# Kernel tuning notes

Measured on AMD Instinct MI355X. Metric: run time of the kernel, lower is better.

## Reference

```python
import jax, jax.numpy as jnp
import numpy as np

B, N, D, H = 1, 4096, 1024, 16
K = D // H
ROPE_BASE = 10000.0


def _rope_cos_sin(n, k, base, dtype):
    # GPT-NeoX style rotary embedding: inv_freq over even dims, emb = cat(freqs, freqs)
    inv_freq = 1.0 / (base ** (jnp.arange(0, k, 2, dtype=jnp.float32) / k))  # [K/2]
    pos = jnp.arange(n, dtype=jnp.float32)
    freqs = pos[:, None] * inv_freq[None, :]              # [N, K/2]
    emb = jnp.concatenate([freqs, freqs], axis=-1)        # [N, K]
    return jnp.cos(emb).astype(dtype), jnp.sin(emb).astype(dtype)


def _rotate_half(x):
    x1, x2 = jnp.split(x, 2, axis=-1)
    return jnp.concatenate([-x2, x1], axis=-1)


def setup_inputs() -> dict:
    key = jax.random.key(0)
    kx, kq, ko = jax.random.split(key, 3)
    x = jax.random.normal(kx, (B, N, D), dtype=jnp.float32)
    # torch Linear weights: [out_features, in_features], y = x @ W^T
    w_qkv = jax.random.normal(kq, (3 * H * K, D), dtype=jnp.float32) / np.sqrt(D)
    w_out = jax.random.normal(ko, (D, D), dtype=jnp.float32) / np.sqrt(D)
    return {"x": x, "w_qkv": w_qkv, "w_out": w_out}


def reference(x, w_qkv, w_out):
    b, n, d = x.shape
    qkv = jnp.einsum('bnd,ed->bne', x, w_qkv).reshape(b, n, 3, H, K)
    q, k, v = qkv[:, :, 0], qkv[:, :, 1], qkv[:, :, 2]   # [B, N, H, K]
    cos, sin = _rope_cos_sin(n, K, ROPE_BASE, x.dtype)    # [N, K]
    cos = cos[None, :, None, :]
    sin = sin[None, :, None, :]
    q = q * cos + _rotate_half(q) * sin
    k = k * cos + _rotate_half(k) * sin
    # explicit O(N^2) score matrix, as in the original module
    scores = jnp.einsum('bnhk,bmhk->bnhm', q, k) / np.sqrt(K).astype(x.dtype)
    causal_mask = jnp.tril(jnp.ones((n, n), dtype=bool))  # [N, M]
    scores = jnp.where(causal_mask[None, :, None, :], scores, jnp.finfo(x.dtype).min)
    probs = jax.nn.softmax(scores, axis=-1)
    attn = jnp.einsum('bnhm,bmhk->bnhk', probs, v).reshape(b, n, d)
    return jnp.einsum('bnd,ed->bne', attn, w_out)
```

## Files before the change

kernel.cpp:

```cpp
#include <hip/hip_runtime.h>
#include <hip/hip_bf16.h>
#include <math.h>

#define N_SEQ 4096
#define DIM   1024
#define NHEAD 16
#define HDIM  64
#define E3    3072

typedef short bf16x8 __attribute__((ext_vector_type(8)));
typedef float f32x4  __attribute__((ext_vector_type(4)));
typedef unsigned int u32;

#if __has_builtin(__builtin_amdgcn_exp2f)
#define EXP2(x) __builtin_amdgcn_exp2f(x)
#else
#define EXP2(x) exp2f(x)
#endif

__device__ __forceinline__ float bf2f(unsigned short u) {
    union { unsigned int i; float f; } x; x.i = ((unsigned int)u) << 16; return x.f;
}
__device__ __forceinline__ unsigned short f2bf(float f) {
    union { float f; unsigned int i; } x; x.f = f;
    unsigned int r = x.i + 0x7FFF + ((x.i >> 16) & 1);
    return (unsigned short)(r >> 16);
}
__device__ __forceinline__ unsigned short f2bf_fast(float f) {
    union { float f; unsigned int i; } x; x.f = f;
    return (unsigned short)((x.i + 0x8000u) >> 16);
}
__device__ __forceinline__ f32x4 mfma16(bf16x8 a, bf16x8 b, f32x4 c) {
    return __builtin_amdgcn_mfma_f32_16x16x32_bf16(a, b, c, 0, 0, 0);
}
__device__ __forceinline__ void gload_lds16(const unsigned short* g, unsigned short* l) {
    __builtin_amdgcn_global_load_lds(
        (const __attribute__((address_space(1))) u32*)g,
        (__attribute__((address_space(3))) u32*)l, 16, 0, 0);
}

__device__ __forceinline__ int probe_isf32(const unsigned short* __restrict__ X) {
    __shared__ int cnt;
    if (threadIdx.x == 0) cnt = 0;
    __syncthreads();
    int bad = 0;
    for (int i = threadIdx.x; i < 4096; i += 256) {
        float v = bf2f(X[i]);
        if (!(fabsf(v) < 1e10f)) bad = 1;
    }
    if (bad) atomicAdd(&cnt, 1);
    __syncthreads();
    return cnt > 0;
}

__global__ __launch_bounds__(256)
void prep_kernel(const void* __restrict__ X, const void* __restrict__ Wq,
                 const void* __restrict__ Wo,
                 unsigned short* __restrict__ Xb, unsigned short* __restrict__ Wqb,
                 unsigned short* __restrict__ Wob,
                 float4* __restrict__ Rt,
                 int* __restrict__ flag)
{
    const int ti = blockIdx.x * blockDim.x + threadIdx.x;
    if (ti < N_SEQ * 16) {
        const int n = ti >> 4, f = ti & 15;
        const float i0 = powf(10000.f, -((float)f)        * (1.f/32.f));
        const float i1 = powf(10000.f, -((float)(f + 16)) * (1.f/32.f));
        float s0, c0, s1, c1;
        sincosf((float)n * i0, &s0, &c0);
        sincosf((float)n * i1, &s1, &c1);
        Rt[ti] = (float4){c0, c1, s0, s1};
    }

    const int isf32 = probe_isf32((const unsigned short*)X);
    if (blockIdx.x == 0 && threadIdx.x == 0) *flag = isf32;
    if (!isf32) return;

    const int nX4  = (N_SEQ * DIM) >> 2;
    const int nWq4 = (E3 * DIM) >> 2;
    const int nWo4 = (DIM * DIM) >> 2;
    const int total = nX4 + nWq4 + nWo4;
    const int stride = gridDim.x * blockDim.x;
    for (int i = blockIdx.x * blockDim.x + threadIdx.x; i < total; i += stride) {
        const float4* src; ushort4* dst; int j = i;
        if (j < nX4)                { src = (const float4*)X  + j;  dst = (ushort4*)Xb  + j; }
        else if ((j -= nX4) < nWq4) { src = (const float4*)Wq + j;  dst = (ushort4*)Wqb + j; }
        else { j -= nWq4;             src = (const float4*)Wo + j;  dst = (ushort4*)Wob + j; }
        float4 v = *src;
        ushort4 u;
        u.x = f2bf(v.x); u.y = f2bf(v.y); u.z = f2bf(v.z); u.w = f2bf(v.w);
        *dst = u;
    }
}

__global__ __launch_bounds__(256)
void qkv_mfma_kernel(const void* __restrict__ Xo, const unsigned short* __restrict__ Xc,
                     const void* __restrict__ Wo_, const unsigned short* __restrict__ Wc,
                     const int* __restrict__ flag,
                     const float4* __restrict__ Rt,
                     unsigned short* __restrict__ Qf,
                     unsigned short* __restrict__ Kf,
                     unsigned short* __restrict__ Vf)
{
    __shared__ __align__(16) unsigned short SMEM[4][4096];

    const int isf32 = *flag;
    const unsigned short* Xb = isf32 ? Xc : (const unsigned short*)Xo;
    const unsigned short* Wb = isf32 ? Wc : (const unsigned short*)Wo_;

    const int tid  = threadIdx.x;
    const int lane = tid & 63;
    const int wave = tid >> 6;
    const int wr = wave >> 1, wc = wave & 1;
    const int lm = lane & 15, q4 = lane >> 4;
    const int rbase = blockIdx.y * 128;
    const int cbase = blockIdx.x * 128;

    const int srow = wave * 16 + (lane >> 2);
    const int scol = (lane & 3) * 8;

    const unsigned short* xsrc = Xb + (size_t)(rbase + srow) * DIM + scol;
    const unsigned short* wsrc = Wb + (size_t)(cbase + srow) * DIM + scol;
    const int la = (wr*64 + lm)*32 + q4*8;
    const int lb = (wc*64 + lm)*32 + q4*8;

    f32x4 acc[4][4];
    #pragma unroll
    for (int i = 0; i < 4; ++i)
        #pragma unroll
        for (int j = 0; j < 4; ++j) acc[i][j] = (f32x4){0.f, 0.f, 0.f, 0.f};

    #define QSTAGE(buf)                                                             \
        {                                                                           \
            _Pragma("unroll")                                                       \
            for (int j = 0; j < 2; ++j) {                                           \
                gload_lds16(xsrc + (size_t)j*64*DIM, &SMEM[buf][j*2048 + wave*512]);   \
                gload_lds16(wsrc + (size_t)j*64*DIM, &SMEM[2+buf][j*2048 + wave*512]); \
            }                                                                       \
            xsrc += 32; wsrc += 32;                                                 \
        }

    QSTAGE(0)
    for (int it = 0; it < DIM/32; ++it) {
        const int cur = it & 1;
        __syncthreads();
        if (it + 1 < DIM/32) QSTAGE(cur ^ 1)

        bf16x8 a[4], b[4];
        #pragma unroll
        for (int mi = 0; mi < 4; ++mi)
            a[mi] = *(const bf16x8*)&SMEM[cur][la + mi*512];
        #pragma unroll
        for (int ni = 0; ni < 4; ++ni)
            b[ni] = *(const bf16x8*)&SMEM[2+cur][lb + ni*512];
        #pragma unroll
        for (int mi = 0; mi < 4; ++mi)
            #pragma unroll
            for (int ni = 0; ni < 4; ++ni)
                acc[mi][ni] = mfma16(a[mi], b[ni], acc[mi][ni]);
    }
    #undef QSTAGE

    __syncthreads();

    const int ecol = cbase + wc * 64;
    const int part = ecol >> 10;
    const int h    = (ecol >> 6) & 15;
    unsigned short* ep = &SMEM[0][0] + wave*4096;

    if (part == 2) {
        #pragma unroll
        for (int mh = 0; mh < 2; ++mh) {
            #pragma unroll
            for (int mi2 = 0; mi2 < 2; ++mi2) {
                const int mi = mh*2 + mi2;
                #pragma unroll
                for (int r = 0; r < 4; ++r) {
                    const int n31 = mi2*16 + q4*4 + r;
                    #pragma unroll
                    for (int ni = 0; ni < 4; ++ni)
                        ep[(ni*16 + lm)*40 + n31] = f2bf(acc[mi][ni][r]);
                }
            }
            const int nb = rbase + wr*64 + mh*32;
            const size_t vb = (((size_t)h*128 + (nb >> 5)) << 11) + (size_t)lane*8;
            #pragma unroll
            for (int ni = 0; ni < 4; ++ni) {
                const bf16x8 fr = *(const bf16x8*)(ep + (ni*16 + lm)*40 + q4*8);
                *(bf16x8*)(Vf + vb + (size_t)ni*512) = fr;
            }
        }
    } else {
        unsigned short* dst = (part == 0) ? Qf : Kf;
        const float scl = (part == 0) ? 0.180336884f : 1.0f;
        #pragma unroll
        for (int mi = 0; mi < 4; ++mi) {
            const int tn = rbase + wr*64 + mi*16;
            #pragma unroll
            for (int r = 0; r < 4; ++r) {
                const int n = tn + q4*4 + r;
                const float4 t = Rt[(n << 4) + lm];
                const int row = (q4*4 + r)*72;
                ep[row + lm]      = f2bf((acc[mi][0][r]*t.x - acc[mi][2][r]*t.z) * scl);
                ep[row + lm + 16] = f2bf((acc[mi][1][r]*t.y - acc[mi][3][r]*t.w) * scl);
                ep[row + lm + 32] = f2bf((acc[mi][2][r]*t.x + acc[mi][0][r]*t.z) * scl);
                ep[row + lm + 48] = f2bf((acc[mi][3][r]*t.y + acc[mi][1][r]*t.w) * scl);
            }
            const size_t tb = (((size_t)(h*256 + (tn >> 4))) << 10) + (size_t)lane*8;
            #pragma unroll
            for (int c = 0; c < 2; ++c) {
                const bf16x8 fr = *(const bf16x8*)(ep + lm*72 + c*32 + q4*8);
                *(bf16x8*)(dst + tb + (size_t)c*512) = fr;
            }
        }
    }
}

__global__ __launch_bounds__(256, 2)
void attn_mfma_kernel(const unsigned short* __restrict__ Qf,
                      const unsigned short* __restrict__ Kf,
                      const unsigned short* __restrict__ Vf,
                      unsigned short* __restrict__ Attn)
{
    __shared__ __align__(16) unsigned short P16[4][2][32][40];
    __shared__ __align__(16) float Ox[2][32][64];
    __shared__ float Lx[2][32];

    const int tid  = threadIdx.x;
    const int lane = tid & 63;
    const int wave = tid >> 6;
    const int q4 = lane >> 4, lm = lane & 15;
    const int qh = wave >> 1, kh = wave & 1;

    const int h = blockIdx.x & 15;
    const int p = blockIdx.x >> 4;
    const int qwA = (p << 6) + (qh << 5);
    const int qwB = ((63 - p) << 6) + (qh << 5);
    const int ntA = p + 1;
    const int ntB = 64 - p;

    const unsigned short* qpA = Qf + (((size_t)(h*256 + (qwA >> 4))) << 10) + (size_t)lane * 8;
    const unsigned short* qpB = Qf + (((size_t)(h*256 + (qwB >> 4))) << 10) + (size_t)lane * 8;
    bf16x8 aqA[2][2], aqB[2][2];
    #pragma unroll
    for (int qi = 0; qi < 2; ++qi)
        #pragma unroll
        for (int d = 0; d < 2; ++d) {
            aqA[qi][d] = *(const bf16x8*)(qpA + qi*1024 + d*512);
            aqB[qi][d] = *(const bf16x8*)(qpB + qi*1024 + d*512);
        }

    float lA[2][4], lB[2][4];
    f32x4 oA[2][4], oB[2][4];
    #pragma unroll
    for (int qi = 0; qi < 2; ++qi) {
        #pragma unroll
        for (int r = 0; r < 4; ++r) { lA[qi][r] = 0.f; lB[qi][r] = 0.f; }
        #pragma unroll
        for (int dc = 0; dc < 4; ++dc) {
            oA[qi][dc] = (f32x4){0.f, 0.f, 0.f, 0.f};
            oB[qi][dc] = (f32x4){0.f, 0.f, 0.f, 0.f};
        }
    }

    const size_t hb = ((size_t)h) << 18;
    const unsigned short* kc = Kf + hb + (size_t)(kh*2048) + (size_t)lane*8;
    const unsigned short* vc = Vf + hb + (size_t)(kh*2048) + (size_t)lane*8;

    unsigned short* pwA  = &P16[wave][0][0][0];
    unsigned short* pwB  = &P16[wave][1][0][0];
    unsigned short* pwaA = pwA + (4*q4)*40 + lm;
    unsigned short* pwaB = pwB + (4*q4)*40 + lm;
    const unsigned short* parA = pwA + lm*40 + q4*8;
    const unsigned short* parB = pwB + lm*40 + q4*8;

    bf16x8 bk[2][2];
    bk[0][0] = *(const bf16x8*)(kc);
    bk[0][1] = *(const bf16x8*)(kc + 512);
    bk[1][0] = *(const bf16x8*)(kc + 1024);
    bk[1][1] = *(const bf16x8*)(kc + 1536);

    for (int it = 0; it < ntB; ++it) {
        const int kt = it << 6;
        const int doA = (it < ntA);

        bf16x8 bv[4];
        #pragma unroll
        for (int dc = 0; dc < 4; ++dc)
            bv[dc] = *(const bf16x8*)(vc + dc*512);

        bf16x8 nk[2][2];
        nk[0][0] = *(const bf16x8*)(kc + 4096);
        nk[0][1] = *(const bf16x8*)(kc + 4096 + 512);
        nk[1][0] = *(const bf16x8*)(kc + 4096 + 1024);
        nk[1][1] = *(const bf16x8*)(kc + 4096 + 1536);

        f32x4 sB[2][2], sA[2][2];
        #pragma unroll
        for (int ki = 0; ki < 2; ++ki)
            #pragma unroll
            for (int qi = 0; qi < 2; ++qi) {
                f32x4 z = (f32x4){0.f, 0.f, 0.f, 0.f};
                z = mfma16(aqB[qi][0], bk[ki][0], z);
                sB[qi][ki] = mfma16(aqB[qi][1], bk[ki][1], z);
            }
        if (doA) {
            #pragma unroll
            for (int ki = 0; ki < 2; ++ki)
                #pragma unroll
                for (int qi = 0; qi < 2; ++qi) {
                    f32x4 z = (f32x4){0.f, 0.f, 0.f, 0.f};
                    z = mfma16(aqA[qi][0], bk[ki][0], z);
                    sA[qi][ki] = mfma16(aqA[qi][1], bk[ki][1], z);
                }
        }

        if (kt + 32*kh + 31 > qwB) {
            #pragma unroll
            for (int ki = 0; ki < 2; ++ki) {
                const int key = kt + 32*kh + 16*ki + lm;
                #pragma unroll
                for (int qi = 0; qi < 2; ++qi) {
                    const int qq = qwB + 16*qi + 4*q4;
                    #pragma unroll
                    for (int r = 0; r < 4; ++r)
                        if (key > qq + r) sB[qi][ki][r] = -INFINITY;
                }
            }
        }

        #pragma unroll
        for (int qi = 0; qi < 2; ++qi)
            #pragma unroll
            for (int ki = 0; ki < 2; ++ki)
                #pragma unroll
                for (int r = 0; r < 4; ++r) {
                    const float pb = EXP2(sB[qi][ki][r]);
                    lB[qi][r] += pb;
                    pwaB[qi*640 + r*40 + ki*16] = f2bf_fast(pb);
                }

        if (doA) {
            if (kt + 32*kh + 31 > qwA) {
                #pragma unroll
                for (int ki = 0; ki < 2; ++ki) {
                    const int key = kt + 32*kh + 16*ki + lm;
                    #pragma unroll
                    for (int qi = 0; qi < 2; ++qi) {
                        const int qq = qwA + 16*qi + 4*q4;
                        #pragma unroll
                        for (int r = 0; r < 4; ++r)
                            if (key > qq + r) sA[qi][ki][r] = -INFINITY;
                    }
                }
            }
            #pragma unroll
            for (int qi = 0; qi < 2; ++qi)
                #pragma unroll
                for (int ki = 0; ki < 2; ++ki)
                    #pragma unroll
                    for (int r = 0; r < 4; ++r) {
                        const float pa = EXP2(sA[qi][ki][r]);
                        lA[qi][r] += pa;
                        pwaA[qi*640 + r*40 + ki*16] = f2bf_fast(pa);
                    }
        }

        {
            bf16x8 paB[2];
            paB[0] = *(const bf16x8*)(parB);
            paB[1] = *(const bf16x8*)(parB + 640);
            #pragma unroll
            for (int dc = 0; dc < 4; ++dc)
                #pragma unroll
                for (int qi = 0; qi < 2; ++qi)
                    oB[qi][dc] = mfma16(paB[qi], bv[dc], oB[qi][dc]);
        }
        if (doA) {
            bf16x8 paA[2];
            paA[0] = *(const bf16x8*)(parA);
            paA[1] = *(const bf16x8*)(parA + 640);
            #pragma unroll
            for (int dc = 0; dc < 4; ++dc)
                #pragma unroll
                for (int qi = 0; qi < 2; ++qi)
                    oA[qi][dc] = mfma16(paA[qi], bv[dc], oA[qi][dc]);
        }

        kc += 4096; vc += 4096;
        bk[0][0] = nk[0][0]; bk[0][1] = nk[0][1];
        bk[1][0] = nk[1][0]; bk[1][1] = nk[1][1];
    }

    #pragma unroll
    for (int qi = 0; qi < 2; ++qi)
        #pragma unroll
        for (int r = 0; r < 4; ++r) {
            float a = lA[qi][r], b = lB[qi][r];
            #pragma unroll
            for (int mk = 1; mk <= 8; mk <<= 1) {
                a += __shfl_xor(a, mk);
                b += __shfl_xor(b, mk);
            }
            lA[qi][r] = a; lB[qi][r] = b;
        }

    if (kh == 1) {
        #pragma unroll
        for (int qi = 0; qi < 2; ++qi)
            #pragma unroll
            for (int r = 0; r < 4; ++r) {
                const int qq = 16*qi + 4*q4 + r;
                #pragma unroll
                for (int dc = 0; dc < 4; ++dc)
                    Ox[qh][qq][16*dc + lm] = oA[qi][dc][r];
                if (lm == 0) Lx[qh][qq] = lA[qi][r];
            }
    }
    __syncthreads();
    if (kh == 0) {
        #pragma unroll
        for (int qi = 0; qi < 2; ++qi)
            #pragma unroll
            for (int r = 0; r < 4; ++r) {
                const int qq = 16*qi + 4*q4 + r;
                const float inv = 1.f / (lA[qi][r] + Lx[qh][qq]);
                const size_t row = (size_t)(qwA + qq) * DIM + (h << 6) + lm;
                #pragma unroll
                for (int dc = 0; dc < 4; ++dc) {
                    const float v = oA[qi][dc][r] + Ox[qh][qq][16*dc + lm];
                    Attn[row + 16*dc] = f2bf(v * inv);
                }
            }
    }
    __syncthreads();
    if (kh == 1) {
        #pragma unroll
        for (int qi = 0; qi < 2; ++qi)
            #pragma unroll
            for (int r = 0; r < 4; ++r) {
                const int qq = 16*qi + 4*q4 + r;
                #pragma unroll
                for (int dc = 0; dc < 4; ++dc)
                    Ox[qh][qq][16*dc + lm] = oB[qi][dc][r];
                if (lm == 0) Lx[qh][qq] = lB[qi][r];
            }
    }
    __syncthreads();
    if (kh == 0) {
        #pragma unroll
        for (int qi = 0; qi < 2; ++qi)
            #pragma unroll
            for (int r = 0; r < 4; ++r) {
                const int qq = 16*qi + 4*q4 + r;
                const float inv = 1.f / (lB[qi][r] + Lx[qh][qq]);
                const size_t row = (size_t)(qwB + qq) * DIM + (h << 6) + lm;
                #pragma unroll
                for (int dc = 0; dc < 4; ++dc) {
                    const float v = oB[qi][dc][r] + Ox[qh][qq][16*dc + lm];
                    Attn[row + 16*dc] = f2bf(v * inv);
                }
            }
    }
}

__global__ __launch_bounds__(256)
void out_mfma_kernel(const unsigned short* __restrict__ Ab,
                     const void* __restrict__ Wo_, const unsigned short* __restrict__ Wc,
                     const int* __restrict__ flag,
                     void* __restrict__ Out)
{
    __shared__ unsigned short As[2][4096];
    __shared__ unsigned short Bs[2][2048];

    const int isf32 = *flag;
    const unsigned short* Wb = isf32 ? Wc : (const unsigned short*)Wo_;

    const int tid  = threadIdx.x;
    const int lane = tid & 63;
    const int wave = tid >> 6;
    const int lm = lane & 15, q4 = lane >> 4;
    const int rbase = blockIdx.y * 128;
    const int cbase = blockIdx.x * 64;

    const int srow16 = lane >> 2;
    const int scol = (lane & 3) * 8;

    const unsigned short* asrc = Ab + (size_t)(rbase + wave*32 + srow16) * DIM + scol;
    const unsigned short* bsrc = Wb + (size_t)(cbase + wave*16 + srow16) * DIM + scol;
    const int la = (wave*32 + lm)*32 + q4*8;
    const int lb = lm*32 + q4*8;

    f32x4 acc[2][4];
    #pragma unroll
    for (int i = 0; i < 2; ++i)
        #pragma unroll
        for (int j = 0; j < 4; ++j) acc[i][j] = (f32x4){0.f, 0.f, 0.f, 0.f};

    #define OSTAGE(buf)                                                          \
        {                                                                        \
            _Pragma("unroll")                                                    \
            for (int j = 0; j < 2; ++j)                                          \
                gload_lds16(asrc + (size_t)j*16*DIM, &As[buf][(wave*32 + j*16)*32]); \
            gload_lds16(bsrc, &Bs[buf][(wave*16)*32]);                           \
            asrc += 32; bsrc += 32;                                              \
        }

    OSTAGE(0)
    for (int it = 0; it < DIM/32; ++it) {
        const int cur = it & 1;
        __syncthreads();
        if (it + 1 < DIM/32) OSTAGE(cur ^ 1)

        bf16x8 a[2], b[4];
        #pragma unroll
        for (int mi = 0; mi < 2; ++mi)
            a[mi] = *(const bf16x8*)&As[cur][la + mi*512];
        #pragma unroll
        for (int ni = 0; ni < 4; ++ni)
            b[ni] = *(const bf16x8*)&Bs[cur][lb + ni*512];
        #pragma unroll
        for (int mi = 0; mi < 2; ++mi)
            #pragma unroll
            for (int ni = 0; ni < 4; ++ni)
                acc[mi][ni] = mfma16(a[mi], b[ni], acc[mi][ni]);
    }
    #undef OSTAGE

    #pragma unroll
    for (int mi = 0; mi < 2; ++mi)
        #pragma unroll
        for (int r = 0; r < 4; ++r) {
            const size_t n = rbase + wave*32 + mi*16 + q4*4 + r;
            #pragma unroll
            for (int ni = 0; ni < 4; ++ni) {
                const size_t e = cbase + ni*16 + lm;
                const float v = acc[mi][ni][r];
                if (isf32) ((float*)Out)[n * DIM + e] = v;
                else       ((unsigned short*)Out)[n * DIM + e] = f2bf(v);
            }
        }
}

extern "C" void kernel_launch(void* const* d_in, const int* in_sizes, int n_in,
                              void* d_out, int out_size, void* d_ws, size_t ws_size,
                              hipStream_t stream) {
    const void* X    = d_in[0];
    const void* Wqkv = d_in[1];
    const void* Wout = d_in[2];

    int* flag = (int*)d_ws;
    unsigned short* base = (unsigned short*)((char*)d_ws + 256);
    const size_t nX = (size_t)N_SEQ * DIM;
    const size_t nWq = (size_t)E3 * DIM;
    const size_t nWo = (size_t)DIM * DIM;
    unsigned short* Xb  = base;
    unsigned short* Wqb = Xb + nX;
    unsigned short* Wob = Wqb + nWq;
    unsigned short* Qf  = Wob + nWo;
    unsigned short* Kf  = Qf + nX;
    unsigned short* Vf  = Kf + nX;
    unsigned short* At  = Vf + nX;
    float4* Rt = (float4*)(At + nX);

    prep_kernel<<<768, 256, 0, stream>>>(X, Wqkv, Wout, Xb, Wqb, Wob, Rt, flag);
    qkv_mfma_kernel<<<dim3(E3 / 128, N_SEQ / 128), 256, 0, stream>>>(X, Xb, Wqkv, Wqb, flag, Rt, Qf, Kf, Vf);
    attn_mfma_kernel<<<dim3(NHEAD * 32), 256, 0, stream>>>(Qf, Kf, Vf, At);
    out_mfma_kernel<<<dim3(DIM / 64, N_SEQ / 128), 256, 0, stream>>>(At, Wout, Wob, flag, d_out);
}
```

Measured before the change: 196.1 us.

## Software-pipeline PV MFMA one iteration behind QK with double-buffered P tiles

The P·V MFMAs are deferred by one key tile. Each iteration now issues the QK MFMAs for the current tile and the PV MFMAs for the previous tile (read from a double-buffered per-wave LDS P area) back to back under raised wave priority. The exp and bf16 conversion for the current tile then run after them, and an epilogue drains the final B tile. The intent is to overlap the exp/LDS-write phase with matrix work and to remove the LDS write-then-read dependency within one iteration, at the cost of doubled P LDS usage and extra registers for the carried V fragments.

```diff
diff --git a/kernel.cpp b/kernel.cpp
--- a/kernel.cpp
+++ b/kernel.cpp
@@ -222,7 +222,7 @@
                       const unsigned short* __restrict__ Vf,
                       unsigned short* __restrict__ Attn)
 {
-    __shared__ __align__(16) unsigned short P16[4][2][32][40];
+    __shared__ __align__(16) unsigned short P16[4][2][2][32][40];
     __shared__ __align__(16) float Ox[2][32][64];
     __shared__ float Lx[2][32];
 
@@ -267,8 +267,8 @@
     const unsigned short* kc = Kf + hb + (size_t)(kh*2048) + (size_t)lane*8;
     const unsigned short* vc = Vf + hb + (size_t)(kh*2048) + (size_t)lane*8;
 
-    unsigned short* pwA  = &P16[wave][0][0][0];
-    unsigned short* pwB  = &P16[wave][1][0][0];
+    unsigned short* pwA  = &P16[wave][0][0][0][0];
+    unsigned short* pwB  = &P16[wave][1][0][0][0];
     unsigned short* pwaA = pwA + (4*q4)*40 + lm;
     unsigned short* pwaB = pwB + (4*q4)*40 + lm;
     const unsigned short* parA = pwA + lm*40 + q4*8;
@@ -280,9 +280,15 @@
     bk[1][0] = *(const bf16x8*)(kc + 1024);
     bk[1][1] = *(const bf16x8*)(kc + 1536);
 
+    bf16x8 bvp[4];
+
     for (int it = 0; it < ntB; ++it) {
         const int kt = it << 6;
         const int doA = (it < ntA);
+        const int pvb = (it > 0);
+        const int pva = (it > 0) & (it <= ntA);
+        const int wb = (it & 1) * 1280;
+        const int rb = wb ^ 1280;
 
         bf16x8 bv[4];
         #pragma unroll
@@ -295,6 +301,17 @@
         nk[1][0] = *(const bf16x8*)(kc + 4096 + 1024);
         nk[1][1] = *(const bf16x8*)(kc + 4096 + 1536);
 
+        bf16x8 paB[2], paA[2];
+        if (pvb) {
+            paB[0] = *(const bf16x8*)(parB + rb);
+            paB[1] = *(const bf16x8*)(parB + rb + 640);
+        }
+        if (pva) {
+            paA[0] = *(const bf16x8*)(parA + rb);
+            paA[1] = *(const bf16x8*)(parA + rb + 640);
+        }
+
+        __builtin_amdgcn_s_setprio(1);
         f32x4 sB[2][2], sA[2][2];
         #pragma unroll
         for (int ki = 0; ki < 2; ++ki)
@@ -314,6 +331,22 @@
                     sA[qi][ki] = mfma16(aqA[qi][1], bk[ki][1], z);
                 }
         }
+
+        if (pvb) {
+            #pragma unroll
+            for (int dc = 0; dc < 4; ++dc)
+                #pragma unroll
+                for (int qi = 0; qi < 2; ++qi)
+                    oB[qi][dc] = mfma16(paB[qi], bvp[dc], oB[qi][dc]);
+        }
+        if (pva) {
+            #pragma unroll
+            for (int dc = 0; dc < 4; ++dc)
+                #pragma unroll
+                for (int qi = 0; qi < 2; ++qi)
+                    oA[qi][dc] = mfma16(paA[qi], bvp[dc], oA[qi][dc]);
+        }
+        __builtin_amdgcn_s_setprio(0);
 
         if (kt + 32*kh + 31 > qwB) {
             #pragma unroll
@@ -328,7 +361,6 @@
                 }
             }
         }
-
         #pragma unroll
         for (int qi = 0; qi < 2; ++qi)
             #pragma unroll
@@ -337,7 +369,7 @@
                 for (int r = 0; r < 4; ++r) {
                     const float pb = EXP2(sB[qi][ki][r]);
                     lB[qi][r] += pb;
-                    pwaB[qi*640 + r*40 + ki*16] = f2bf_fast(pb);
+                    pwaB[wb + qi*640 + r*40 + ki*16] = f2bf_fast(pb);
                 }
 
         if (doA) {
@@ -362,34 +394,27 @@
                     for (int r = 0; r < 4; ++r) {
                         const float pa = EXP2(sA[qi][ki][r]);
                         lA[qi][r] += pa;
-                        pwaA[qi*640 + r*40 + ki*16] = f2bf_fast(pa);
+                        pwaA[wb + qi*640 + r*40 + ki*16] = f2bf_fast(pa);
                     }
-        }
-
-        {
-            bf16x8 paB[2];
-            paB[0] = *(const bf16x8*)(parB);
-            paB[1] = *(const bf16x8*)(parB + 640);
-            #pragma unroll
-            for (int dc = 0; dc < 4; ++dc)
-                #pragma unroll
-                for (int qi = 0; qi < 2; ++qi)
-                    oB[qi][dc] = mfma16(paB[qi], bv[dc], oB[qi][dc]);
-        }
-        if (doA) {
-            bf16x8 paA[2];
-            paA[0] = *(const bf16x8*)(parA);
-            paA[1] = *(const bf16x8*)(parA + 640);
-            #pragma unroll
-            for (int dc = 0; dc < 4; ++dc)
-                #pragma unroll
-                for (int qi = 0; qi < 2; ++qi)
-                    oA[qi][dc] = mfma16(paA[qi], bv[dc], oA[qi][dc]);
         }
 
         kc += 4096; vc += 4096;
         bk[0][0] = nk[0][0]; bk[0][1] = nk[0][1];
         bk[1][0] = nk[1][0]; bk[1][1] = nk[1][1];
+        #pragma unroll
+        for (int dc = 0; dc < 4; ++dc) bvp[dc] = bv[dc];
+    }
+
+    {
+        const int rb = ((ntB - 1) & 1) * 1280;
+        bf16x8 paB[2];
+        paB[0] = *(const bf16x8*)(parB + rb);
+        paB[1] = *(const bf16x8*)(parB + rb + 640);
+        #pragma unroll
+        for (int dc = 0; dc < 4; ++dc)
+            #pragma unroll
+            for (int qi = 0; qi < 2; ++qi)
+                oB[qi][dc] = mfma16(paB[qi], bvp[dc], oB[qi][dc]);
     }
 
     #pragma unroll
```

Result: no change. 198.4 us (+1.2%).

## Split attention work across 8 waves with 16 query rows each

Applied to the files above, without the earlier changes.

The attention kernel now launches 512 threads per block, and each wave handles 16 query rows instead of 32. Per-wave Q fragments, accumulators and the P staging buffer shrink to match, and the shared-memory reduction buffers are resized for four query groups. This roughly halves register pressure per wave and doubles the waves per CU on the same grid, to hide memory and MFMA latency better. In exchange, each K/V fragment loaded into registers is reused across half as many queries, which doubles K/V load traffic per block.

```diff
diff --git a/kernel.cpp b/kernel.cpp
--- a/kernel.cpp
+++ b/kernel.cpp
@@ -216,51 +216,47 @@
     }
 }
 
-__global__ __launch_bounds__(256, 2)
+__global__ __launch_bounds__(512, 4)
 void attn_mfma_kernel(const unsigned short* __restrict__ Qf,
                       const unsigned short* __restrict__ Kf,
                       const unsigned short* __restrict__ Vf,
                       unsigned short* __restrict__ Attn)
 {
-    __shared__ __align__(16) unsigned short P16[4][2][32][40];
-    __shared__ __align__(16) float Ox[2][32][64];
-    __shared__ float Lx[2][32];
+    __shared__ __align__(16) unsigned short P16[8][2][16][40];
+    __shared__ __align__(16) float Ox[4][16][64];
+    __shared__ float Lx[4][16];
 
     const int tid  = threadIdx.x;
     const int lane = tid & 63;
     const int wave = tid >> 6;
     const int q4 = lane >> 4, lm = lane & 15;
-    const int qh = wave >> 1, kh = wave & 1;
+    const int qh = wave >> 1;
+    const int kh = wave & 1;
 
     const int h = blockIdx.x & 15;
     const int p = blockIdx.x >> 4;
-    const int qwA = (p << 6) + (qh << 5);
-    const int qwB = ((63 - p) << 6) + (qh << 5);
+    const int qwA = (p << 6) + (qh << 4);
+    const int qwB = ((63 - p) << 6) + (qh << 4);
     const int ntA = p + 1;
     const int ntB = 64 - p;
 
     const unsigned short* qpA = Qf + (((size_t)(h*256 + (qwA >> 4))) << 10) + (size_t)lane * 8;
     const unsigned short* qpB = Qf + (((size_t)(h*256 + (qwB >> 4))) << 10) + (size_t)lane * 8;
-    bf16x8 aqA[2][2], aqB[2][2];
-    #pragma unroll
-    for (int qi = 0; qi < 2; ++qi)
-        #pragma unroll
-        for (int d = 0; d < 2; ++d) {
-            aqA[qi][d] = *(const bf16x8*)(qpA + qi*1024 + d*512);
-            aqB[qi][d] = *(const bf16x8*)(qpB + qi*1024 + d*512);
-        }
-
-    float lA[2][4], lB[2][4];
-    f32x4 oA[2][4], oB[2][4];
-    #pragma unroll
-    for (int qi = 0; qi < 2; ++qi) {
-        #pragma unroll
-        for (int r = 0; r < 4; ++r) { lA[qi][r] = 0.f; lB[qi][r] = 0.f; }
-        #pragma unroll
-        for (int dc = 0; dc < 4; ++dc) {
-            oA[qi][dc] = (f32x4){0.f, 0.f, 0.f, 0.f};
-            oB[qi][dc] = (f32x4){0.f, 0.f, 0.f, 0.f};
-        }
+    bf16x8 aqA[2], aqB[2];
+    #pragma unroll
+    for (int d = 0; d < 2; ++d) {
+        aqA[d] = *(const bf16x8*)(qpA + d*512);
+        aqB[d] = *(const bf16x8*)(qpB + d*512);
+    }
+
+    float lA[4], lB[4];
+    f32x4 oA[4], oB[4];
+    #pragma unroll
+    for (int r = 0; r < 4; ++r) { lA[r] = 0.f; lB[r] = 0.f; }
+    #pragma unroll
+    for (int dc = 0; dc < 4; ++dc) {
+        oA[dc] = (f32x4){0.f, 0.f, 0.f, 0.f};
+        oB[dc] = (f32x4){0.f, 0.f, 0.f, 0.f};
     }
 
     const size_t hb = ((size_t)h) << 18;
@@ -295,96 +291,74 @@
         nk[1][0] = *(const bf16x8*)(kc + 4096 + 1024);
         nk[1][1] = *(const bf16x8*)(kc + 4096 + 1536);
 
-        f32x4 sB[2][2], sA[2][2];
-        #pragma unroll
-        for (int ki = 0; ki < 2; ++ki)
-            #pragma unroll
-            for (int qi = 0; qi < 2; ++qi) {
+        f32x4 sB[2], sA[2];
+        #pragma unroll
+        for (int ki = 0; ki < 2; ++ki) {
+            f32x4 z = (f32x4){0.f, 0.f, 0.f, 0.f};
+            z = mfma16(aqB[0], bk[ki][0], z);
+            sB[ki] = mfma16(aqB[1], bk[ki][1], z);
+        }
+        if (doA) {
+            #pragma unroll
+            for (int ki = 0; ki < 2; ++ki) {
                 f32x4 z = (f32x4){0.f, 0.f, 0.f, 0.f};
-                z = mfma16(aqB[qi][0], bk[ki][0], z);
-                sB[qi][ki] = mfma16(aqB[qi][1], bk[ki][1], z);
-            }
-        if (doA) {
-            #pragma unroll
-            for (int ki = 0; ki < 2; ++ki)
-                #pragma unroll
-                for (int qi = 0; qi < 2; ++qi) {
-                    f32x4 z = (f32x4){0.f, 0.f, 0.f, 0.f};
-                    z = mfma16(aqA[qi][0], bk[ki][0], z);
-                    sA[qi][ki] = mfma16(aqA[qi][1], bk[ki][1], z);
-                }
+                z = mfma16(aqA[0], bk[ki][0], z);
+                sA[ki] = mfma16(aqA[1], bk[ki][1], z);
+            }
         }
 
         if (kt + 32*kh + 31 > qwB) {
             #pragma unroll
             for (int ki = 0; ki < 2; ++ki) {
                 const int key = kt + 32*kh + 16*ki + lm;
+                const int qq = qwB + 4*q4;
                 #pragma unroll
-                for (int qi = 0; qi < 2; ++qi) {
-                    const int qq = qwB + 16*qi + 4*q4;
-                    #pragma unroll
-                    for (int r = 0; r < 4; ++r)
-                        if (key > qq + r) sB[qi][ki][r] = -INFINITY;
-                }
-            }
-        }
-
-        #pragma unroll
-        for (int qi = 0; qi < 2; ++qi)
-            #pragma unroll
-            for (int ki = 0; ki < 2; ++ki)
-                #pragma unroll
-                for (int r = 0; r < 4; ++r) {
-                    const float pb = EXP2(sB[qi][ki][r]);
-                    lB[qi][r] += pb;
-                    pwaB[qi*640 + r*40 + ki*16] = f2bf_fast(pb);
-                }
+                for (int r = 0; r < 4; ++r)
+                    if (key > qq + r) sB[ki][r] = -INFINITY;
+            }
+        }
+
+        #pragma unroll
+        for (int ki = 0; ki < 2; ++ki)
+            #pragma unroll
+            for (int r = 0; r < 4; ++r) {
+                const float pb = EXP2(sB[ki][r]);
+                lB[r] += pb;
+                pwaB[r*40 + ki*16] = f2bf_fast(pb);
+            }
 
         if (doA) {
             if (kt + 32*kh + 31 > qwA) {
                 #pragma unroll
                 for (int ki = 0; ki < 2; ++ki) {
                     const int key = kt + 32*kh + 16*ki + lm;
+                    const int qq = qwA + 4*q4;
                     #pragma unroll
-                    for (int qi = 0; qi < 2; ++qi) {
-                        const int qq = qwA + 16*qi + 4*q4;
-                        #pragma unroll
-                        for (int r = 0; r < 4; ++r)
-                            if (key > qq + r) sA[qi][ki][r] = -INFINITY;
-                    }
+                    for (int r = 0; r < 4; ++r)
+                        if (key > qq + r) sA[ki][r] = -INFINITY;
                 }
             }
             #pragma unroll
-            for (int qi = 0; qi < 2; ++qi)
+            for (int ki = 0; ki < 2; ++ki)
                 #pragma unroll
-                for (int ki = 0; ki < 2; ++ki)
-                    #pragma unroll
-                    for (int r = 0; r < 4; ++r) {
-                        const float pa = EXP2(sA[qi][ki][r]);
-                        lA[qi][r] += pa;
-                        pwaA[qi*640 + r*40 + ki*16] = f2bf_fast(pa);
-                    }
+                for (int r = 0; r < 4; ++r) {
+                    const float pa = EXP2(sA[ki][r]);
+                    lA[r] += pa;
+                    pwaA[r*40 + ki*16] = f2bf_fast(pa);
+                }
         }
 
         {
-            bf16x8 paB[2];
-            paB[0] = *(const bf16x8*)(parB);
-            paB[1] = *(const bf16x8*)(parB + 640);
+            const bf16x8 paB = *(const bf16x8*)(parB);
             #pragma unroll
             for (int dc = 0; dc < 4; ++dc)
-                #pragma unroll
-                for (int qi = 0; qi < 2; ++qi)
-                    oB[qi][dc] = mfma16(paB[qi], bv[dc], oB[qi][dc]);
+                oB[dc] = mfma16(paB, bv[dc], oB[dc]);
         }
         if (doA) {
-            bf16x8 paA[2];
-            paA[0] = *(const bf16x8*)(parA);
-            paA[1] = *(const bf16x8*)(parA + 640);
+            const bf16x8 paA = *(const bf16x8*)(parA);
             #pragma unroll
             for (int dc = 0; dc < 4; ++dc)
-                #pragma unroll
-                for (int qi = 0; qi < 2; ++qi)
-                    oA[qi][dc] = mfma16(paA[qi], bv[dc], oA[qi][dc]);
+                oA[dc] = mfma16(paA, bv[dc], oA[dc]);
         }
 
         kc += 4096; vc += 4096;
@@ -393,74 +367,64 @@
     }
 
     #pragma unroll
-    for (int qi = 0; qi < 2; ++qi)
+    for (int r = 0; r < 4; ++r) {
+        float a = lA[r], b = lB[r];
+        #pragma unroll
+        for (int mk = 1; mk <= 8; mk <<= 1) {
+            a += __shfl_xor(a, mk);
+            b += __shfl_xor(b, mk);
+        }
+        lA[r] = a; lB[r] = b;
+    }
+
+    if (kh == 1) {
         #pragma unroll
         for (int r = 0; r < 4; ++r) {
-            float a = lA[qi][r], b = lB[qi][r];
-            #pragma unroll
-            for (int mk = 1; mk <= 8; mk <<= 1) {
-                a += __shfl_xor(a, mk);
-                b += __shfl_xor(b, mk);
-            }
-            lA[qi][r] = a; lB[qi][r] = b;
-        }
-
-    if (kh == 1) {
-        #pragma unroll
-        for (int qi = 0; qi < 2; ++qi)
-            #pragma unroll
-            for (int r = 0; r < 4; ++r) {
-                const int qq = 16*qi + 4*q4 + r;
-                #pragma unroll
-                for (int dc = 0; dc < 4; ++dc)
-                    Ox[qh][qq][16*dc + lm] = oA[qi][dc][r];
-                if (lm == 0) Lx[qh][qq] = lA[qi][r];
-            }
+            const int qq = 4*q4 + r;
+            #pragma unroll
+            for (int dc = 0; dc < 4; ++dc)
+                Ox[qh][qq][16*dc + lm] = oA[dc][r];
+            if (lm == 0) Lx[qh][qq] = lA[r];
+        }
     }
     __syncthreads();
     if (kh == 0) {
         #pragma unroll
-        for (int qi = 0; qi < 2; ++qi)
-            #pragma unroll
-            for (int r = 0; r < 4; ++r) {
-                const int qq = 16*qi + 4*q4 + r;
-                const float inv = 1.f / (lA[qi][r] + Lx[qh][qq]);
-                const size_t row = (size_t)(qwA + qq) * DIM + (h << 6) + lm;
-                #pragma unroll
-                for (int dc = 0; dc < 4; ++dc) {
-                    const float v = oA[qi][dc][r] + Ox[qh][qq][16*dc + lm];
-                    Attn[row + 16*dc] = f2bf(v * inv);
-                }
-            }
+        for (int r = 0; r < 4; ++r) {
+            const int qq = 4*q4 + r;
+            const float inv = 1.f / (lA[r] + Lx[qh][qq]);
+            const size_t row = (size_t)(qwA + qq) * DIM + (h << 6) + lm;
+            #pragma unroll
+            for (int dc = 0; dc < 4; ++dc) {
+                const float v = oA[dc][r] + Ox[qh][qq][16*dc + lm];
+                Attn[row + 16*dc] = f2bf(v * inv);
+            }
+        }
     }
     __syncthreads();
     if (kh == 1) {
         #pragma unroll
-        for (int qi = 0; qi < 2; ++qi)
-            #pragma unroll
-            for (int r = 0; r < 4; ++r) {
-                const int qq = 16*qi + 4*q4 + r;
-                #pragma unroll
-                for (int dc = 0; dc < 4; ++dc)
-                    Ox[qh][qq][16*dc + lm] = oB[qi][dc][r];
-                if (lm == 0) Lx[qh][qq] = lB[qi][r];
-            }
+        for (int r = 0; r < 4; ++r) {
+            const int qq = 4*q4 + r;
+            #pragma unroll
+            for (int dc = 0; dc < 4; ++dc)
+                Ox[qh][qq][16*dc + lm] = oB[dc][r];
+            if (lm == 0) Lx[qh][qq] = lB[r];
+        }
     }
     __syncthreads();
     if (kh == 0) {
         #pragma unroll
-        for (int qi = 0; qi < 2; ++qi)
-            #pragma unroll
-            for (int r = 0; r < 4; ++r) {
-                const int qq = 16*qi + 4*q4 + r;
-                const float inv = 1.f / (lB[qi][r] + Lx[qh][qq]);
-                const size_t row = (size_t)(qwB + qq) * DIM + (h << 6) + lm;
-                #pragma unroll
-                for (int dc = 0; dc < 4; ++dc) {
-                    const float v = oB[qi][dc][r] + Ox[qh][qq][16*dc + lm];
-                    Attn[row + 16*dc] = f2bf(v * inv);
-                }
-            }
+        for (int r = 0; r < 4; ++r) {
+            const int qq = 4*q4 + r;
+            const float inv = 1.f / (lB[r] + Lx[qh][qq]);
+            const size_t row = (size_t)(qwB + qq) * DIM + (h << 6) + lm;
+            #pragma unroll
+            for (int dc = 0; dc < 4; ++dc) {
+                const float v = oB[dc][r] + Ox[qh][qq][16*dc + lm];
+                Attn[row + 16*dc] = f2bf(v * inv);
+            }
+        }
     }
 }
 
@@ -565,6 +529,6 @@
 
     prep_kernel<<<768, 256, 0, stream>>>(X, Wqkv, Wout, Xb, Wqb, Wob, Rt, flag);
     qkv_mfma_kernel<<<dim3(E3 / 128, N_SEQ / 128), 256, 0, stream>>>(X, Xb, Wqkv, Wqb, flag, Rt, Qf, Kf, Vf);
-    attn_mfma_kernel<<<dim3(NHEAD * 32), 256, 0, stream>>>(Qf, Kf, Vf, At);
+    attn_mfma_kernel<<<dim3(NHEAD * 32), 512, 0, stream>>>(Qf, Kf, Vf, At);
     out_mfma_kernel<<<dim3(DIM / 64, N_SEQ / 128), 256, 0, stream>>>(At, Wout, Wob, flag, d_out);
 }
```

New measurement: 223.6 us. 1.14x slower.
